# Kernel optimization log

Measured on AMD Instinct MI355X. Metric: run time of the kernel, lower is better.

## Reference

```python
import jax, jax.numpy as jnp
import numpy as np

D = 2048      # hidden dim
H = 16        # heads
BSZ = 4       # batch
L = 2048      # seq len
BASE_DT = 0.1


def setup_inputs() -> dict:
    key = jax.random.key(0)
    ks = jax.random.split(key, 9)
    s = 1.0 / np.sqrt(D)
    x = jax.random.normal(ks[0], (BSZ, L, D), dtype=jnp.float32)
    v = jax.random.normal(ks[1], (BSZ, L, D), dtype=jnp.float32)
    force = jax.random.normal(ks[2], (BSZ, L, D), dtype=jnp.float32)
    WA = jax.random.normal(ks[3], (D, D), dtype=jnp.float32) * s
    bA = jnp.zeros((D,), dtype=jnp.float32)
    WB = jax.random.normal(ks[4], (D, D), dtype=jnp.float32) * s
    bB = jnp.zeros((D,), dtype=jnp.float32)
    Wdt = jax.random.normal(ks[5], (D, D), dtype=jnp.float32) * s
    bdt = jnp.zeros((D,), dtype=jnp.float32)
    # base_dt_scales buffer: 1.5**head_index, repeated head_dim times
    scales = jnp.repeat(1.5 ** jnp.arange(H, dtype=jnp.float32), D // H)
    return {"x": x, "v": v, "force": force, "WA": WA, "bA": bA,
            "WB": WB, "bB": bB, "Wdt": Wdt, "bdt": bdt, "scales": scales}


def _combine(e1, e2):
    # associative op for v_t = a_t * v_{t-1} + b_t ; e1 is the earlier element
    a1, b1 = e1
    a2, b2 = e2
    return a1 * a2, a2 * b1 + b2


def reference(x, v, force, WA, bA, WB, bB, Wdt, bdt, scales):
    # x is LayerNorm-ed in the original but the result is unused; v is unused.
    A = jax.nn.sigmoid(force @ WA + bA)                      # [B, L, D] in (0,1)
    dt = jax.nn.softplus(force @ Wdt + bdt) * BASE_DT * scales  # per-head dt scaling
    B_val = (force @ WB + bB) * dt
    # parallel associative scan over the sequence axis: v_t = A_t v_{t-1} + B_t
    _, v_seq = jax.lax.associative_scan(_combine, (A, B_val), axis=1)
    # second scan has A=1 -> plain prefix sum
    x_seq = jnp.cumsum(v_seq * dt, axis=1)
    return x_seq, v_seq
```

## Files before the change

kernel.cpp:

```cpp
#include <hip/hip_runtime.h>
#include <hip/hip_bf16.h>
#include <cstdint>
#include <cstddef>

#define D_DIM 2048
#define L_SEQ 2048
#define B_SZ 4
#define M_ROWS (B_SZ * L_SEQ)
#define NT_COLS (3 * D_DIM)
#define NCH 16
#define CHUNK (L_SEQ / NCH)

typedef __bf16 bf16_t;
typedef bf16_t bf16x4 __attribute__((ext_vector_type(4)));
typedef bf16_t bf16x8 __attribute__((ext_vector_type(8)));
typedef float f32x4 __attribute__((ext_vector_type(4)));

__device__ __forceinline__ void gl_lds16(const void* g, void* l) {
    __builtin_amdgcn_global_load_lds(
        (const __attribute__((address_space(1))) unsigned int*)g,
        (__attribute__((address_space(3))) unsigned int*)l, 16, 0, 0);
}

__global__ __launch_bounds__(256) void cvt_bf16_kernel(
    const float* __restrict__ in, bf16_t* __restrict__ out, int n8)
{
    int i = blockIdx.x * 256 + threadIdx.x;
    if (i >= n8) return;
    float4 f0 = ((const float4*)in)[2 * i];
    float4 f1 = ((const float4*)in)[2 * i + 1];
    bf16x8 o;
    o[0] = (bf16_t)f0.x; o[1] = (bf16_t)f0.y; o[2] = (bf16_t)f0.z; o[3] = (bf16_t)f0.w;
    o[4] = (bf16_t)f1.x; o[5] = (bf16_t)f1.y; o[6] = (bf16_t)f1.z; o[7] = (bf16_t)f1.w;
    ((bf16x8*)out)[i] = o;
}

__global__ __launch_bounds__(256) void transpose_w_kernel(
    const float* __restrict__ W0, const float* __restrict__ W1,
    const float* __restrict__ W2, bf16_t* __restrict__ Wt)
{
    __shared__ float tile[32][33];
    const float* W = (blockIdx.z == 0) ? W0 : (blockIdx.z == 1) ? W1 : W2;
    bf16_t* dst = Wt + (size_t)blockIdx.z * D_DIM * D_DIM;
    int j0 = blockIdx.x * 32, k0 = blockIdx.y * 32;
    int tx = threadIdx.x, ty = threadIdx.y;
#pragma unroll
    for (int i = 0; i < 4; i++) {
        int k = k0 + ty + i * 8;
        tile[ty + i * 8][tx] = W[(size_t)k * D_DIM + j0 + tx];
    }
    __syncthreads();
#pragma unroll
    for (int i = 0; i < 4; i++) {
        int j = j0 + ty + i * 8;
        dst[(size_t)j * D_DIM + k0 + tx] = (bf16_t)tile[tx][ty + i * 8];
    }
}

__global__ __launch_bounds__(256) void gemm_fused_kernel(
    const bf16_t* __restrict__ Abf,
    const bf16_t* __restrict__ Wt,
    const float* __restrict__ bA, const float* __restrict__ bdt,
    const float* __restrict__ bB, const float* __restrict__ scales,
    float* __restrict__ outA,
    float* __restrict__ outDT,
    float* __restrict__ outB)
{
    __shared__ bf16_t lds_a[128 * 32];
    __shared__ bf16_t lds_b[128 * 32];

    const int bm0 = blockIdx.x * 128;
    const int bn0 = blockIdx.y * 128;
    const int t = threadIdx.x;
    const int lane = t & 63, w = t >> 6;
    const int wr = (w >> 1) * 64;
    const int wc = (w & 1) * 64;

    f32x4 acc[4][4] = {};

    const int lin0 = t, lin1 = t + 256;
    const int ar0 = lin0 >> 2, ac0 = (lin0 & 3) * 8;
    const int ar1 = lin1 >> 2, ac1 = (lin1 & 3) * 8;
    const int frow = lane & 15;
    const int fk = (lane >> 4) * 8;

    for (int k0 = 0; k0 < D_DIM; k0 += 32) {
        gl_lds16(Abf + (size_t)(bm0 + ar0) * D_DIM + k0 + ac0, lds_a + w * 512);
        gl_lds16(Abf + (size_t)(bm0 + ar1) * D_DIM + k0 + ac1, lds_a + 2048 + w * 512);
        gl_lds16(Wt  + (size_t)(bn0 + ar0) * D_DIM + k0 + ac0, lds_b + w * 512);
        gl_lds16(Wt  + (size_t)(bn0 + ar1) * D_DIM + k0 + ac1, lds_b + 2048 + w * 512);
        __syncthreads();

        bf16x8 af[4], bfr[4];
#pragma unroll
        for (int m = 0; m < 4; m++)
            af[m] = *(const bf16x8*)&lds_a[(wr + m * 16 + frow) * 32 + fk];
#pragma unroll
        for (int n = 0; n < 4; n++)
            bfr[n] = *(const bf16x8*)&lds_b[(wc + n * 16 + frow) * 32 + fk];
#pragma unroll
        for (int m = 0; m < 4; m++)
#pragma unroll
            for (int n = 0; n < 4; n++)
                acc[m][n] = __builtin_amdgcn_mfma_f32_16x16x32_bf16(
                    af[m], bfr[n], acc[m][n], 0, 0, 0);
        __syncthreads();
    }

    const int seg = bn0 >> 11;
    const int dbase = (bn0 & 2047) + wc + (lane & 15);
    const int rowbase = bm0 + wr + ((lane >> 4) << 2);
#pragma unroll
    for (int m = 0; m < 4; m++) {
#pragma unroll
        for (int n = 0; n < 4; n++) {
            int d = dbase + n * 16;
#pragma unroll
            for (int r = 0; r < 4; r++) {
                int gm = rowbase + m * 16 + r;
                size_t idx = (size_t)gm * D_DIM + d;
                float val = acc[m][n][r];
                if (seg == 0) {
                    outA[idx] = 1.0f / (1.0f + __expf(-(val + bA[d])));
                } else if (seg == 1) {
                    float xx = val + bdt[d];
                    float sp = xx > 0.f ? xx + log1pf(__expf(-xx)) : log1pf(__expf(xx));
                    outDT[idx] = sp * 0.1f * scales[d];
                } else {
                    outB[idx] = val + bB[d];
                }
            }
        }
    }
}

__global__ __launch_bounds__(256) void scan_pass1_kernel(
    const float* __restrict__ Aarr, const float* __restrict__ Braw,
    const float* __restrict__ dtv, float4* __restrict__ agg)
{
    int pp = blockIdx.x * 256 + threadIdx.x;
    int dp = (pp & 1023) << 1;
    int c = (pp >> 10) & (NCH - 1);
    int b = pp >> 14;
    size_t base = ((size_t)(b * L_SEQ + c * CHUNK)) * D_DIM + dp;
    float P0 = 1.f, R0 = 0.f, U0 = 0.f, W0 = 0.f;
    float P1 = 1.f, R1 = 0.f, U1 = 0.f, W1 = 0.f;
#pragma unroll 4
    for (int tt = 0; tt < CHUNK; tt++) {
        size_t idx = base + (size_t)tt * D_DIM;
        float2 a2  = *(const float2*)&Aarr[idx];
        float2 rb2 = *(const float2*)&Braw[idx];
        float2 dt2 = *(const float2*)&dtv[idx];
        float bv0 = rb2.x * dt2.x, bv1 = rb2.y * dt2.y;
        float da0 = dt2.x * a2.x,  da1 = dt2.y * a2.y;
        R0 = da0 * P0 + R0;  W0 = da0 * U0 + dt2.x * bv0 + W0;
        U0 = a2.x * U0 + bv0;  P0 = a2.x * P0;
        R1 = da1 * P1 + R1;  W1 = da1 * U1 + dt2.y * bv1 + W1;
        U1 = a2.y * U1 + bv1;  P1 = a2.y * P1;
    }
    int ch = ((b * NCH + c) << 11) + dp;
    agg[ch]     = make_float4(P0, R0, U0, W0);
    agg[ch + 1] = make_float4(P1, R1, U1, W1);
}

__global__ __launch_bounds__(256) void scan_pass2_kernel(
    const float4* __restrict__ agg, float2* __restrict__ pre)
{
    int tid = blockIdx.x * 256 + threadIdx.x;
    int d = tid & (D_DIM - 1);
    int b = tid >> 11;
    float v = 0.f, x = 0.f;
#pragma unroll
    for (int c = 0; c < NCH; c++) {
        int i = ((b * NCH + c) << 11) + d;
        float4 g = agg[i];
        pre[i] = make_float2(v, x);
        float vn = g.x * v + g.z;
        x = g.y * v + x + g.w;
        v = vn;
    }
}

__global__ __launch_bounds__(256) void scan_pass3_kernel(
    const float* __restrict__ dtv, const float2* __restrict__ pre,
    float* __restrict__ xout, float* __restrict__ vout)
{
    int pp = blockIdx.x * 256 + threadIdx.x;
    int dp = (pp & 1023) << 1;
    int c = (pp >> 10) & (NCH - 1);
    int b = pp >> 14;
    int ch = ((b * NCH + c) << 11) + dp;
    float4 pv = *(const float4*)&pre[ch];
    float v0 = pv.x, x0 = pv.y, v1 = pv.z, x1 = pv.w;
    size_t base = ((size_t)(b * L_SEQ + c * CHUNK)) * D_DIM + dp;
#pragma unroll 4
    for (int tt = 0; tt < CHUNK; tt++) {
        size_t idx = base + (size_t)tt * D_DIM;
        float2 a2  = *(const float2*)&xout[idx];
        float2 rb2 = *(const float2*)&vout[idx];
        float2 dt2 = *(const float2*)&dtv[idx];
        v0 = a2.x * v0 + rb2.x * dt2.x;
        x0 = x0 + v0 * dt2.x;
        v1 = a2.y * v1 + rb2.y * dt2.y;
        x1 = x1 + v1 * dt2.y;
        *(float2*)&vout[idx] = make_float2(v0, v1);
        *(float2*)&xout[idx] = make_float2(x0, x1);
    }
}

extern "C" void kernel_launch(void* const* d_in, const int* in_sizes, int n_in,
                              void* d_out, int out_size, void* d_ws, size_t ws_size,
                              hipStream_t stream) {
    const float* force  = (const float*)d_in[2];
    const float* WA     = (const float*)d_in[3];
    const float* bA     = (const float*)d_in[4];
    const float* WB     = (const float*)d_in[5];
    const float* bB     = (const float*)d_in[6];
    const float* Wdt    = (const float*)d_in[7];
    const float* bdt    = (const float*)d_in[8];
    const float* scales = (const float*)d_in[9];

    float* xout = (float*)d_out;
    float* vout = xout + (size_t)M_ROWS * D_DIM;

    char* ws = (char*)d_ws;
    bf16_t* fbf = (bf16_t*)ws;
    bf16_t* wt  = (bf16_t*)(ws + (size_t)33554432);
    float*  dtv = (float*)(ws + (size_t)33554432 + 25165824);
    float4* agg = (float4*)(ws + (size_t)33554432 + 25165824 + 67108864);
    float2* pre = (float2*)(ws + (size_t)33554432 + 25165824 + 67108864 + 2097152);

    {
        int n8 = M_ROWS * D_DIM / 8;
        cvt_bf16_kernel<<<n8 / 256, 256, 0, stream>>>(force, fbf, n8);
    }
    {
        dim3 grid(D_DIM / 32, D_DIM / 32, 3), block(32, 8);
        transpose_w_kernel<<<grid, block, 0, stream>>>(WA, Wdt, WB, wt);
    }
    {
        dim3 grid(M_ROWS / 128, NT_COLS / 128);
        gemm_fused_kernel<<<grid, 256, 0, stream>>>(fbf, wt, bA, bdt, bB, scales,
                                                    xout, dtv, vout);
    }
    scan_pass1_kernel<<<(B_SZ * NCH * D_DIM / 2) / 256, 256, 0, stream>>>(xout, vout, dtv, agg);
    scan_pass2_kernel<<<(B_SZ * D_DIM) / 256, 256, 0, stream>>>(agg, pre);
    scan_pass3_kernel<<<(B_SZ * NCH * D_DIM / 2) / 256, 256, 0, stream>>>(dtv, pre, xout, vout);
}
```

Before: 493.7 us.

## Double GEMM K-tile to 64 with XOR-swizzled LDS and hoisted epilogue biases

The fused GEMM now stages a 64-wide K slice per iteration instead of 32, which halves the number of barrier pairs and loop iterations. LDS columns are XOR-swizzled by row so that the 16-byte fragment reads avoid bank conflicts. The epilogue branches on the segment once and loads bias and scale values into registers before the store loops, rather than re-reading them per element. LDS use per block doubles to 32 KB, which may lower occupancy, and there is still no double buffering.

```diff
diff --git a/kernel.cpp b/kernel.cpp
--- a/kernel.cpp
+++ b/kernel.cpp
@@ -12,7 +12,6 @@
 #define CHUNK (L_SEQ / NCH)
 
 typedef __bf16 bf16_t;
-typedef bf16_t bf16x4 __attribute__((ext_vector_type(4)));
 typedef bf16_t bf16x8 __attribute__((ext_vector_type(8)));
 typedef float f32x4 __attribute__((ext_vector_type(4)));
 
@@ -66,8 +65,8 @@
     float* __restrict__ outDT,
     float* __restrict__ outB)
 {
-    __shared__ bf16_t lds_a[128 * 32];
-    __shared__ bf16_t lds_b[128 * 32];
+    __shared__ bf16_t lds_a[128 * 64];
+    __shared__ bf16_t lds_b[128 * 64];
 
     const int bm0 = blockIdx.x * 128;
     const int bn0 = blockIdx.y * 128;
@@ -78,26 +77,43 @@
 
     f32x4 acc[4][4] = {};
 
-    const int lin0 = t, lin1 = t + 256;
-    const int ar0 = lin0 >> 2, ac0 = (lin0 & 3) * 8;
-    const int ar1 = lin1 >> 2, ac1 = (lin1 & 3) * 8;
+    const int srow = t >> 3;
+    const int scol = (((t & 7) ^ ((t >> 3) & 7)) << 3);
     const int frow = lane & 15;
-    const int fk = (lane >> 4) * 8;
-
-    for (int k0 = 0; k0 < D_DIM; k0 += 32) {
-        gl_lds16(Abf + (size_t)(bm0 + ar0) * D_DIM + k0 + ac0, lds_a + w * 512);
-        gl_lds16(Abf + (size_t)(bm0 + ar1) * D_DIM + k0 + ac1, lds_a + 2048 + w * 512);
-        gl_lds16(Wt  + (size_t)(bn0 + ar0) * D_DIM + k0 + ac0, lds_b + w * 512);
-        gl_lds16(Wt  + (size_t)(bn0 + ar1) * D_DIM + k0 + ac1, lds_b + 2048 + w * 512);
+    const int q = lane >> 4;
+    const int fx7 = frow & 7;
+    const int lof0 = frow * 64 + (((q) ^ fx7) << 3);
+    const int lof1 = frow * 64 + (((4 + q) ^ fx7) << 3);
+
+    for (int k0 = 0; k0 < D_DIM; k0 += 64) {
+#pragma unroll
+        for (int j = 0; j < 4; j++) {
+            gl_lds16(Abf + (size_t)(bm0 + j * 32 + srow) * D_DIM + k0 + scol,
+                     lds_a + j * 2048 + w * 512);
+            gl_lds16(Wt  + (size_t)(bn0 + j * 32 + srow) * D_DIM + k0 + scol,
+                     lds_b + j * 2048 + w * 512);
+        }
         __syncthreads();
 
         bf16x8 af[4], bfr[4];
 #pragma unroll
         for (int m = 0; m < 4; m++)
-            af[m] = *(const bf16x8*)&lds_a[(wr + m * 16 + frow) * 32 + fk];
+            af[m] = *(const bf16x8*)&lds_a[(wr + m * 16) * 64 + lof0];
 #pragma unroll
         for (int n = 0; n < 4; n++)
-            bfr[n] = *(const bf16x8*)&lds_b[(wc + n * 16 + frow) * 32 + fk];
+            bfr[n] = *(const bf16x8*)&lds_b[(wc + n * 16) * 64 + lof0];
+#pragma unroll
+        for (int m = 0; m < 4; m++)
+#pragma unroll
+            for (int n = 0; n < 4; n++)
+                acc[m][n] = __builtin_amdgcn_mfma_f32_16x16x32_bf16(
+                    af[m], bfr[n], acc[m][n], 0, 0, 0);
+#pragma unroll
+        for (int m = 0; m < 4; m++)
+            af[m] = *(const bf16x8*)&lds_a[(wr + m * 16) * 64 + lof1];
+#pragma unroll
+        for (int n = 0; n < 4; n++)
+            bfr[n] = *(const bf16x8*)&lds_b[(wc + n * 16) * 64 + lof1];
 #pragma unroll
         for (int m = 0; m < 4; m++)
 #pragma unroll
@@ -110,27 +126,48 @@
     const int seg = bn0 >> 11;
     const int dbase = (bn0 & 2047) + wc + (lane & 15);
     const int rowbase = bm0 + wr + ((lane >> 4) << 2);
-#pragma unroll
-    for (int m = 0; m < 4; m++) {
-#pragma unroll
-        for (int n = 0; n < 4; n++) {
-            int d = dbase + n * 16;
-#pragma unroll
-            for (int r = 0; r < 4; r++) {
-                int gm = rowbase + m * 16 + r;
-                size_t idx = (size_t)gm * D_DIM + d;
-                float val = acc[m][n][r];
-                if (seg == 0) {
-                    outA[idx] = 1.0f / (1.0f + __expf(-(val + bA[d])));
-                } else if (seg == 1) {
-                    float xx = val + bdt[d];
+
+    if (seg == 0) {
+        float bias[4];
+#pragma unroll
+        for (int n = 0; n < 4; n++) bias[n] = bA[dbase + n * 16];
+#pragma unroll
+        for (int m = 0; m < 4; m++)
+#pragma unroll
+            for (int n = 0; n < 4; n++)
+#pragma unroll
+                for (int r = 0; r < 4; r++) {
+                    size_t idx = (size_t)(rowbase + m * 16 + r) * D_DIM + dbase + n * 16;
+                    outA[idx] = 1.0f / (1.0f + __expf(-(acc[m][n][r] + bias[n])));
+                }
+    } else if (seg == 1) {
+        float bias[4], sc[4];
+#pragma unroll
+        for (int n = 0; n < 4; n++) { bias[n] = bdt[dbase + n * 16]; sc[n] = scales[dbase + n * 16]; }
+#pragma unroll
+        for (int m = 0; m < 4; m++)
+#pragma unroll
+            for (int n = 0; n < 4; n++)
+#pragma unroll
+                for (int r = 0; r < 4; r++) {
+                    size_t idx = (size_t)(rowbase + m * 16 + r) * D_DIM + dbase + n * 16;
+                    float xx = acc[m][n][r] + bias[n];
                     float sp = xx > 0.f ? xx + log1pf(__expf(-xx)) : log1pf(__expf(xx));
-                    outDT[idx] = sp * 0.1f * scales[d];
-                } else {
-                    outB[idx] = val + bB[d];
+                    outDT[idx] = sp * 0.1f * sc[n];
                 }
-            }
-        }
+    } else {
+        float bias[4];
+#pragma unroll
+        for (int n = 0; n < 4; n++) bias[n] = bB[dbase + n * 16];
+#pragma unroll
+        for (int m = 0; m < 4; m++)
+#pragma unroll
+            for (int n = 0; n < 4; n++)
+#pragma unroll
+                for (int r = 0; r < 4; r++) {
+                    size_t idx = (size_t)(rowbase + m * 16 + r) * D_DIM + dbase + n * 16;
+                    outB[idx] = acc[m][n][r] + bias[n];
+                }
     }
 }
 
```

Measured after the change: 457.3 us. -7.4%, faster.
